# Kernel tuning notes

Measured on AMD Instinct MI355X. Metric: run time of the kernel, lower is better.

## Reference

```python
import jax, jax.numpy as jnp
import numpy as np

N_NODES = 50000
N_EDGES = 1600000
IN_DIM, HIDDEN, OUT_DIM = 128, 128, 64


def setup_inputs() -> dict:
    key = jax.random.key(0)
    ks = jax.random.split(key, 8)
    x = jax.random.normal(ks[0], (N_NODES, IN_DIM), dtype=jnp.float32)
    edge_index = jax.random.randint(ks[1], (2, N_EDGES), 0, N_NODES, dtype=jnp.int64)
    # SAGEConv params: lin_l applied to aggregated neighbors (with bias),
    # lin_r applied to root/self features (no bias) -- PyG defaults.
    def lin_init(k, fan_in, fan_out):
        bound = 1.0 / np.sqrt(fan_in)
        return jax.random.uniform(k, (fan_in, fan_out), jnp.float32, -bound, bound)
    W1_l = lin_init(ks[2], IN_DIM, HIDDEN)
    W1_r = lin_init(ks[3], IN_DIM, HIDDEN)
    b1 = jnp.zeros((HIDDEN,), jnp.float32)
    W2_l = lin_init(ks[4], HIDDEN, OUT_DIM)
    W2_r = lin_init(ks[5], HIDDEN, OUT_DIM)
    b2 = jnp.zeros((OUT_DIM,), jnp.float32)
    return {"x": x, "edge_index": edge_index, "W1_l": W1_l, "W1_r": W1_r,
            "b1": b1, "W2_l": W2_l, "W2_r": W2_r, "b2": b2}


def _sage_conv(h, src, dst, n_nodes, W_l, W_r, b):
    # gather messages from source nodes, mean-aggregate at destinations
    msg = h[src]                                              # [E, D]
    agg_sum = jax.ops.segment_sum(msg, dst, num_segments=n_nodes)
    deg = jax.ops.segment_sum(jnp.ones((src.shape[0],), h.dtype), dst,
                              num_segments=n_nodes)
    agg_mean = agg_sum / jnp.maximum(deg, 1.0)[:, None]       # [N, D]
    return agg_mean @ W_l + h @ W_r + b


def reference(x, edge_index, W1_l, W1_r, b1, W2_l, W2_r, b2):
    n = x.shape[0]
    src, dst = edge_index[0], edge_index[1]
    h = jax.nn.relu(_sage_conv(x, src, dst, n, W1_l, W1_r, b1))
    return _sage_conv(h, src, dst, n, W2_l, W2_r, b2)
```

## Files before the change

kernel.cpp:

```cpp
#include <hip/hip_runtime.h>

#define NN 50000
#define NE 1600000
#define BSTRIDE 96
#define BNODES 50
#define C_BKT 1000
#define P1_BLKS 256
#define P1_CHUNK 6250
#define ZID 50000
#define XCVT_BLKS 1563
#define WCVT_BLKS 48
#define PP_PREP (XCVT_BLKS + WCVT_BLKS)
#define RGRP 3128

typedef __bf16 bf16x8 __attribute__((ext_vector_type(8)));
typedef float  f32x4  __attribute__((ext_vector_type(4)));
typedef float  f32x2  __attribute__((ext_vector_type(2)));

__device__ __forceinline__ float bfLo(uint u) { union { uint i; float f; } v; v.i = u << 16; return v.f; }
__device__ __forceinline__ float bfHi(uint u) { union { uint i; float f; } v; v.i = u & 0xffff0000u; return v.f; }
__device__ __forceinline__ ushort f2bf(float f) {
    union { float f; uint i; } v; v.f = f;
    uint r = v.i + 0x7fffu + ((v.i >> 16) & 1u);
    return (ushort)(r >> 16);
}
__device__ __forceinline__ uint pack2(float a, float b) {
    return (uint)f2bf(a) | ((uint)f2bf(b) << 16);
}
__device__ __forceinline__ bf16x8 load8(const ushort* p) {
    union { uint4 u; bf16x8 b; } v; v.u = *(const uint4*)p; return v.b;
}

#define ACC8(u) { a0 += bfLo(u.x); a1 += bfHi(u.x); a2 += bfLo(u.y); a3 += bfHi(u.y); \
                  a4 += bfLo(u.z); a5 += bfHi(u.z); a6 += bfLo(u.w); a7 += bfHi(u.w); }

#define CVA(u, o) { f32x2 p0 = __builtin_amdgcn_cvt_pk_f32_fp8((int)(u), 0); \
                    f32x2 p1 = __builtin_amdgcn_cvt_pk_f32_fp8((int)(u), 1); \
                    a[(o)+0] += p0.x; a[(o)+1] += p0.y; a[(o)+2] += p1.x; a[(o)+3] += p1.y; }
#define ACCF8(v) { CVA((v).x, 0); CVA((v).y, 4); CVA((v).z, 8); CVA((v).w, 12); }

__device__ __forceinline__ int pkOff(int n, int k) {
    return (((n >> 4) * 4 + (k >> 5)) * 512) + (((k >> 3) & 3) * 128) + ((n & 15) * 8) + (k & 7);
}

__global__ __launch_bounds__(1024) void k_pp(
    const float4* __restrict__ x, ushort* __restrict__ xbp, uint* __restrict__ xf8,
    const float* __restrict__ W1l, const float* __restrict__ W1r,
    const float* __restrict__ W2l, const float* __restrict__ W2r,
    ushort* __restrict__ T1l, ushort* __restrict__ T1r,
    ushort* __restrict__ T2l, ushort* __restrict__ T2r,
    const int* __restrict__ src, const int* __restrict__ dst,
    uint* __restrict__ cells, uint* __restrict__ offc, ushort* __restrict__ hW) {
    __shared__ uint hist[C_BKT + 1];
    __shared__ uint part[128];
    const int b = blockIdx.x;
    const int tid = threadIdx.x;
    if (b < XCVT_BLKS) {
        int i = b * 1024 + tid;
        if (i < NN * 128 / 4) {
            float4 v = x[i];
            int r = i >> 5, k0 = (i & 31) * 4;
            ushort4 o; o.x = f2bf(v.x); o.y = f2bf(v.y); o.z = f2bf(v.z); o.w = f2bf(v.w);
            *(ushort4*)(xbp + pkOff(r, k0)) = o;
            uint rr = (uint)__builtin_amdgcn_cvt_pk_fp8_f32(v.x, v.y, 0, 0);
            rr = (uint)__builtin_amdgcn_cvt_pk_fp8_f32(v.z, v.w, (int)rr, 1);
            xf8[i] = rr;
        } else if (b == XCVT_BLKS - 1) {
            if (tid >= 512 && tid < 544) xf8[(size_t)ZID * 32 + (tid - 512)] = 0;
            else if (tid >= 544 && tid < 576) ((uint*)hW)[(size_t)ZID * 32 + (tid - 544)] = 0;
        }
    } else if (b < PP_PREP) {
        int i = (b - XCVT_BLKS) * 1024 + tid;
        if (i < 16384) {
            int k = i >> 7, n = i & 127; T1l[pkOff(n, k)] = f2bf(W1l[i]);
        } else if (i < 32768) {
            int j = i - 16384; int k = j >> 7, n = j & 127; T1r[pkOff(n, k)] = f2bf(W1r[j]);
        } else if (i < 40960) {
            int j = i - 32768; int k = j >> 6, n = j & 63;  T2l[pkOff(n, k)] = f2bf(W2l[j]);
        } else {
            int j = i - 40960; int k = j >> 6, n = j & 63;  T2r[pkOff(n, k)] = f2bf(W2r[j]);
        }
    } else {
        const int b2 = b - PP_PREP;
        for (int i = tid; i < C_BKT; i += 1024) hist[i] = 0;
        __syncthreads();
        const int beg = b2 * P1_CHUNK;
        for (int i = beg + tid; i < beg + P1_CHUNK; i += 1024)
            atomicAdd(&hist[dst[i] / BNODES], 1);
        __syncthreads();
        if (tid < 125) {
            uint s = 0;
            #pragma unroll
            for (int k = 0; k < 8; k++) {
                uint t = hist[tid * 8 + k];
                hist[tid * 8 + k] = s;
                s += t;
            }
            part[tid] = s;
        }
        __syncthreads();
        if (tid == 0) {
            uint run = 0;
            for (int t = 0; t < 125; t++) { uint tmp = part[t]; part[t] = run; run += tmp; }
        }
        __syncthreads();
        if (tid < 125) {
            uint bs = part[tid];
            if (bs) {
                #pragma unroll
                for (int k = 0; k < 8; k++) hist[tid * 8 + k] += bs;
            }
        }
        __syncthreads();
        for (int c = tid; c < C_BKT; c += 1024) {
            uint st = hist[c];
            uint en = (c == C_BKT - 1) ? (uint)P1_CHUNK : hist[c + 1];
            offc[(size_t)c * P1_BLKS + b2] = st | ((en - st) << 16);
        }
        __syncthreads();
        uint* myCells = cells + (size_t)b2 * P1_CHUNK;
        for (int i = beg + tid; i < beg + P1_CHUNK; i += 1024) {
            int d = dst[i];
            int s = src[i];
            int c = d / BNODES;
            uint p = atomicAdd(&hist[c], 1);
            myCells[p] = ((uint)(d - c * BNODES) << 16) | (uint)s;
        }
    }
}

__global__ __launch_bounds__(512) void k_pagg(
    const uint* __restrict__ cells, const uint* __restrict__ offc,
    const uchar* __restrict__ xf8, ushort* __restrict__ col,
    int* __restrict__ deg, ushort* __restrict__ aggp) {
    __shared__ uint hist[BNODES];
    __shared__ __align__(16) ushort colS[BNODES * BSTRIDE];
    const int bid = blockIdx.x;
    const int c = (bid & 7) * 125 + (bid >> 3);
    const int tid = threadIdx.x;
    if (tid < BNODES) hist[tid] = 0;
    __syncthreads();
    {
        const int b = tid >> 1, sub = tid & 1;
        uint v = offc[(size_t)c * P1_BLKS + b];
        int st = (int)(v & 0xFFFF), n = (int)(v >> 16);
        const uint* cell = cells + (size_t)b * P1_CHUNK + st;
        for (int j = sub; j < n; j += 2) {
            uint e = cell[j];
            int dl = e >> 16;
            uint p = atomicAdd(&hist[dl], 1);
            if (p < BSTRIDE) colS[dl * BSTRIDE + p] = (ushort)(e & 0xFFFF);
        }
    }
    __syncthreads();
    const int nodeBase = c * BNODES;
    if (tid < BNODES) {
        deg[nodeBase + tid] = (int)hist[tid];
        int dd = min((int)hist[tid], BSTRIDE);
        int dr = (dd + 7) & ~7;
        for (int j = dd; j < dr; j++) colS[tid * BSTRIDE + j] = (ushort)ZID;
    }
    __syncthreads();
    {
        uint4* cg = (uint4*)(col + (size_t)nodeBase * BSTRIDE);
        const uint4* cs = (const uint4*)colS;
        for (int i = tid; i < BNODES * BSTRIDE / 8; i += 512) cg[i] = cs[i];
    }
    const int wave = tid >> 6, lane = tid & 63;
    const int q = lane >> 3;
    const int cc = lane & 7;
    for (int ln = wave; ln < BNODES; ln += 8) {
        int d = (int)hist[ln];
        int dd = min(d, BSTRIDE);
        int nb = ((dd + 7) & ~7) >> 3;
        const int base = ln * BSTRIDE;
        float a[16];
        #pragma unroll
        for (int i = 0; i < 16; i++) a[i] = 0.f;
        int t = 0;
        for (; t + 4 <= nb; t += 4) {
            int s0 = (int)colS[base + t * 8 + q];
            int s1 = (int)colS[base + t * 8 + 8 + q];
            int s2 = (int)colS[base + t * 8 + 16 + q];
            int s3 = (int)colS[base + t * 8 + 24 + q];
            uint4 u0 = *(const uint4*)(xf8 + (size_t)s0 * 128 + cc * 16);
            uint4 u1 = *(const uint4*)(xf8 + (size_t)s1 * 128 + cc * 16);
            uint4 u2 = *(const uint4*)(xf8 + (size_t)s2 * 128 + cc * 16);
            uint4 u3 = *(const uint4*)(xf8 + (size_t)s3 * 128 + cc * 16);
            ACCF8(u0); ACCF8(u1); ACCF8(u2); ACCF8(u3);
        }
        for (; t < nb; t++) {
            int s = (int)colS[base + t * 8 + q];
            uint4 u = *(const uint4*)(xf8 + (size_t)s * 128 + cc * 16);
            ACCF8(u);
        }
        #pragma unroll
        for (int m = 8; m < 64; m <<= 1) {
            #pragma unroll
            for (int i = 0; i < 16; i++) a[i] += __shfl_xor(a[i], m);
        }
        if (q == 0) {
            int node = nodeBase + ln;
            float inv = 1.f / fmaxf((float)d, 1.f);
            int basep = ((node >> 4) * 4 + (cc >> 1)) * 512 + ((cc & 1) * 2) * 128 + (node & 15) * 8;
            uint4 o;
            o.x = pack2(a[0] * inv, a[1] * inv);
            o.y = pack2(a[2] * inv, a[3] * inv);
            o.z = pack2(a[4] * inv, a[5] * inv);
            o.w = pack2(a[6] * inv, a[7] * inv);
            *(uint4*)(aggp + basep) = o;
            o.x = pack2(a[8] * inv, a[9] * inv);
            o.y = pack2(a[10] * inv, a[11] * inv);
            o.z = pack2(a[12] * inv, a[13] * inv);
            o.w = pack2(a[14] * inv, a[15] * inv);
            *(uint4*)(aggp + basep + 128) = o;
        }
    }
}

#define PAD1 136
__global__ __launch_bounds__(256) void k_gemm12(
    const ushort* __restrict__ aggp, const ushort* __restrict__ xbp,
    const ushort* __restrict__ T1l, const ushort* __restrict__ T1r,
    const ushort* __restrict__ T2l, const ushort* __restrict__ T2r,
    const float* __restrict__ b1, const float* __restrict__ b2,
    ushort* __restrict__ hW, float* __restrict__ outp) {
    __shared__ ushort hS[2][16 * PAD1];
    const int lane = threadIdx.x & 63;
    const int wave = threadIdx.x >> 6;
    const int s = wave >> 1;
    const int ch = wave & 1;
    const int quad = lane >> 4, r16 = lane & 15;
    const int row0 = blockIdx.x * 32 + s * 16;
    const int g = blockIdx.x * 2 + s;
    ushort* myS = &hS[s][0];

    f32x4 acc[4];
    #pragma unroll
    for (int nt = 0; nt < 4; nt++) acc[nt] = (f32x4){0.f, 0.f, 0.f, 0.f};
    #pragma unroll
    for (int kt = 0; kt < 4; kt++) {
        bf16x8 aAgg = load8(aggp + (size_t)(g * 4 + kt) * 512 + lane * 8);
        bf16x8 aXb  = load8(xbp  + (size_t)(g * 4 + kt) * 512 + lane * 8);
        #pragma unroll
        for (int nt = 0; nt < 4; nt++) {
            const int tile = ((ch * 4 + nt) * 4 + kt) * 512 + lane * 8;
            acc[nt] = __builtin_amdgcn_mfma_f32_16x16x32_bf16(aAgg, load8(T1l + tile), acc[nt], 0, 0, 0);
            acc[nt] = __builtin_amdgcn_mfma_f32_16x16x32_bf16(aXb,  load8(T1r + tile), acc[nt], 0, 0, 0);
        }
    }
    #pragma unroll
    for (int nt = 0; nt < 4; nt++) {
        int cc = ch * 64 + nt * 16 + r16;
        float bv = b1[cc];
        #pragma unroll
        for (int i = 0; i < 4; i++)
            myS[(quad * 4 + i) * PAD1 + cc] = f2bf(fmaxf(acc[nt][i] + bv, 0.f));
    }
    __syncthreads();

    f32x4 acc2[2], acc3[2];
    #pragma unroll
    for (int nt = 0; nt < 2; nt++) {
        acc2[nt] = (f32x4){0.f, 0.f, 0.f, 0.f};
        acc3[nt] = (f32x4){0.f, 0.f, 0.f, 0.f};
    }
    #pragma unroll
    for (int kt = 0; kt < 4; kt++) {
        bf16x8 ah = load8(&myS[r16 * PAD1 + kt * 32 + quad * 8]);
        #pragma unroll
        for (int nt = 0; nt < 2; nt++) {
            const int tile = ((ch * 2 + nt) * 4 + kt) * 512 + lane * 8;
            acc2[nt] = __builtin_amdgcn_mfma_f32_16x16x32_bf16(ah, load8(T2l + tile), acc2[nt], 0, 0, 0);
            acc3[nt] = __builtin_amdgcn_mfma_f32_16x16x32_bf16(ah, load8(T2r + tile), acc3[nt], 0, 0, 0);
        }
    }
    #pragma unroll
    for (int nt = 0; nt < 2; nt++) {
        int cc = ch * 32 + nt * 16 + r16;
        float bv = b2[cc];
        #pragma unroll
        for (int i = 0; i < 4; i++) {
            int rr = row0 + quad * 4 + i;
            if (rr < NN) {
                hW[(size_t)rr * 64 + cc] = f2bf(acc2[nt][i]);
                outp[(size_t)rr * 64 + cc] = acc3[nt][i] + bv;
            }
        }
    }
}

__global__ __launch_bounds__(256) void k_agg64f(
    const ushort* __restrict__ hW, const ushort* __restrict__ col,
    const int* __restrict__ deg, const float* __restrict__ outp,
    float* __restrict__ out) {
    __shared__ __align__(16) ushort colB[4 * BSTRIDE];
    const int tid = threadIdx.x;
    const int node0 = blockIdx.x * 4;
    if (tid < 48) {
        const uint4* cg = (const uint4*)(col + (size_t)node0 * BSTRIDE);
        *(uint4*)&colB[tid * 8] = cg[tid];
    }
    __syncthreads();
    const int wave = tid >> 6, lane = tid & 63;
    const int node = node0 + wave;
    const int q = lane >> 3;
    const int c = lane & 7;
    const int base = wave * BSTRIDE;
    int d = deg[node];
    int dd = min(d, BSTRIDE);
    int nb = ((dd + 7) & ~7) >> 3;
    float a0=0.f,a1=0.f,a2=0.f,a3=0.f,a4=0.f,a5=0.f,a6=0.f,a7=0.f;
    int t = 0;
    for (; t + 4 <= nb; t += 4) {
        int s0 = (int)colB[base + t * 8 + q];
        int s1 = (int)colB[base + t * 8 + 8 + q];
        int s2 = (int)colB[base + t * 8 + 16 + q];
        int s3 = (int)colB[base + t * 8 + 24 + q];
        uint4 u0 = *(const uint4*)(hW + (size_t)s0 * 64 + c * 8);
        uint4 u1 = *(const uint4*)(hW + (size_t)s1 * 64 + c * 8);
        uint4 u2 = *(const uint4*)(hW + (size_t)s2 * 64 + c * 8);
        uint4 u3 = *(const uint4*)(hW + (size_t)s3 * 64 + c * 8);
        ACC8(u0); ACC8(u1); ACC8(u2); ACC8(u3);
    }
    for (; t < nb; t++) {
        int s = (int)colB[base + t * 8 + q];
        uint4 u = *(const uint4*)(hW + (size_t)s * 64 + c * 8);
        ACC8(u);
    }
    #pragma unroll
    for (int m = 8; m < 64; m <<= 1) {
        a0 += __shfl_xor(a0, m); a1 += __shfl_xor(a1, m);
        a2 += __shfl_xor(a2, m); a3 += __shfl_xor(a3, m);
        a4 += __shfl_xor(a4, m); a5 += __shfl_xor(a5, m);
        a6 += __shfl_xor(a6, m); a7 += __shfl_xor(a7, m);
    }
    if (q == 0) {
        float inv = 1.f / fmaxf((float)d, 1.f);
        float4 p0 = *(const float4*)(outp + (size_t)node * 64 + c * 8);
        float4 p1 = *(const float4*)(outp + (size_t)node * 64 + c * 8 + 4);
        float4 o;
        o.x = a0 * inv + p0.x; o.y = a1 * inv + p0.y;
        o.z = a2 * inv + p0.z; o.w = a3 * inv + p0.w;
        *(float4*)(out + (size_t)node * 64 + c * 8) = o;
        o.x = a4 * inv + p1.x; o.y = a5 * inv + p1.y;
        o.z = a6 * inv + p1.z; o.w = a7 * inv + p1.w;
        *(float4*)(out + (size_t)node * 64 + c * 8 + 4) = o;
    }
}

extern "C" void kernel_launch(void* const* d_in, const int* in_sizes, int n_in,
                              void* d_out, int out_size, void* d_ws, size_t ws_size,
                              hipStream_t stream) {
    const float* x   = (const float*)d_in[0];
    const int*   ei  = (const int*)d_in[1];
    const float* W1l = (const float*)d_in[2];
    const float* W1r = (const float*)d_in[3];
    const float* b1  = (const float*)d_in[4];
    const float* W2l = (const float*)d_in[5];
    const float* W2r = (const float*)d_in[6];
    const float* b2  = (const float*)d_in[7];
    float* out = (float*)d_out;

    const int* src = ei;
    const int* dst = ei + NE;

    char* w = (char*)d_ws;
    ushort* col   = (ushort*)w;                  w += (size_t)NN * BSTRIDE * 2;
    int* deg      = (int*)w;                     w += (size_t)50048 * 4;
    uint* offc    = (uint*)w;                    w += (size_t)C_BKT * P1_BLKS * 4;
    ushort* xbp   = (ushort*)w;                  w += (size_t)RGRP * 2048 * 2;
    ushort* T1l   = (ushort*)w;                  w += 128 * 128 * 2;
    ushort* T1r   = (ushort*)w;                  w += 128 * 128 * 2;
    ushort* T2l   = (ushort*)w;                  w += 64 * 128 * 2;
    ushort* T2r   = (ushort*)w;                  w += 64 * 128 * 2;
    ushort* aggp  = (ushort*)w;                  w += (size_t)RGRP * 2048 * 2;
    ushort* hW    = (ushort*)w;                  w += (size_t)(NN + 16) * 64 * 2;
    float* outp   = (float*)w;                   w += (size_t)NN * 64 * 4;
    uchar* xf8    = (uchar*)w;                   w += (size_t)(NN + 16) * 128;
    uint* cells   = (uint*)w;                    w += (size_t)NE * 4;

    k_pp<<<PP_PREP + P1_BLKS, 1024, 0, stream>>>(
        (const float4*)x, xbp, (uint*)xf8, W1l, W1r, W2l, W2r,
        T1l, T1r, T2l, T2r, src, dst, cells, offc, hW);

    k_pagg<<<C_BKT, 512, 0, stream>>>(cells, offc, xf8, col, deg, aggp);

    k_gemm12<<<(NN + 31) / 32, 256, 0, stream>>>(aggp, xbp, T1l, T1r, T2l, T2r, b1, b2, hW, outp);

    k_agg64f<<<NN / 4, 256, 0, stream>>>(hW, col, deg, outp, out);
}
```

Baseline: 196.0 us.

## Halve aggregation bucket size and use packed f32x2 accumulation

Buckets now cover 25 destination nodes instead of 50, giving 2000 aggregation blocks of 256 threads instead of 1000 blocks of 512. Each thread now scans one partition's cell range serially instead of two threads splitting it. The bucket prefix scan is widened to match. Separately, the bf16 and fp8 accumulators in both aggregation kernels are rewritten as f32x2 vector adds so the compiler can emit packed FP32 adds. The trade is more blocks and a larger offset table against less work per block and fewer add instructions.

```diff
diff --git a/kernel.cpp b/kernel.cpp
--- a/kernel.cpp
+++ b/kernel.cpp
@@ -3,8 +3,8 @@
 #define NN 50000
 #define NE 1600000
 #define BSTRIDE 96
-#define BNODES 50
-#define C_BKT 1000
+#define BNODES 25
+#define C_BKT 2000
 #define P1_BLKS 256
 #define P1_CHUNK 6250
 #define ZID 50000
@@ -19,6 +19,9 @@
 
 __device__ __forceinline__ float bfLo(uint u) { union { uint i; float f; } v; v.i = u << 16; return v.f; }
 __device__ __forceinline__ float bfHi(uint u) { union { uint i; float f; } v; v.i = u & 0xffff0000u; return v.f; }
+__device__ __forceinline__ f32x2 bfPair(uint u) {
+    union { uint i[2]; f32x2 f; } v; v.i[0] = u << 16; v.i[1] = u & 0xffff0000u; return v.f;
+}
 __device__ __forceinline__ ushort f2bf(float f) {
     union { float f; uint i; } v; v.f = f;
     uint r = v.i + 0x7fffu + ((v.i >> 16) & 1u);
@@ -31,13 +34,12 @@
     union { uint4 u; bf16x8 b; } v; v.u = *(const uint4*)p; return v.b;
 }
 
-#define ACC8(u) { a0 += bfLo(u.x); a1 += bfHi(u.x); a2 += bfLo(u.y); a3 += bfHi(u.y); \
-                  a4 += bfLo(u.z); a5 += bfHi(u.z); a6 += bfLo(u.w); a7 += bfHi(u.w); }
+#define ACC8P(u) { b0 += bfPair(u.x); b1 += bfPair(u.y); b2 += bfPair(u.z); b3 += bfPair(u.w); }
 
 #define CVA(u, o) { f32x2 p0 = __builtin_amdgcn_cvt_pk_f32_fp8((int)(u), 0); \
                     f32x2 p1 = __builtin_amdgcn_cvt_pk_f32_fp8((int)(u), 1); \
-                    a[(o)+0] += p0.x; a[(o)+1] += p0.y; a[(o)+2] += p1.x; a[(o)+3] += p1.y; }
-#define ACCF8(v) { CVA((v).x, 0); CVA((v).y, 4); CVA((v).z, 8); CVA((v).w, 12); }
+                    a[(o)] += p0; a[(o)+1] += p1; }
+#define ACCF8(v) { CVA((v).x, 0); CVA((v).y, 2); CVA((v).z, 4); CVA((v).w, 6); }
 
 __device__ __forceinline__ int pkOff(int n, int k) {
     return (((n >> 4) * 4 + (k >> 5)) * 512) + (((k >> 3) & 3) * 128) + ((n & 15) * 8) + (k & 7);
@@ -52,7 +54,7 @@
     const int* __restrict__ src, const int* __restrict__ dst,
     uint* __restrict__ cells, uint* __restrict__ offc, ushort* __restrict__ hW) {
     __shared__ uint hist[C_BKT + 1];
-    __shared__ uint part[128];
+    __shared__ uint part[250];
     const int b = blockIdx.x;
     const int tid = threadIdx.x;
     if (b < XCVT_BLKS) {
@@ -88,7 +90,7 @@
         for (int i = beg + tid; i < beg + P1_CHUNK; i += 1024)
             atomicAdd(&hist[dst[i] / BNODES], 1);
         __syncthreads();
-        if (tid < 125) {
+        if (tid < 250) {
             uint s = 0;
             #pragma unroll
             for (int k = 0; k < 8; k++) {
@@ -101,10 +103,10 @@
         __syncthreads();
         if (tid == 0) {
             uint run = 0;
-            for (int t = 0; t < 125; t++) { uint tmp = part[t]; part[t] = run; run += tmp; }
-        }
-        __syncthreads();
-        if (tid < 125) {
+            for (int t = 0; t < 250; t++) { uint tmp = part[t]; part[t] = run; run += tmp; }
+        }
+        __syncthreads();
+        if (tid < 250) {
             uint bs = part[tid];
             if (bs) {
                 #pragma unroll
@@ -129,23 +131,22 @@
     }
 }
 
-__global__ __launch_bounds__(512) void k_pagg(
+__global__ __launch_bounds__(256) void k_pagg(
     const uint* __restrict__ cells, const uint* __restrict__ offc,
     const uchar* __restrict__ xf8, ushort* __restrict__ col,
     int* __restrict__ deg, ushort* __restrict__ aggp) {
     __shared__ uint hist[BNODES];
     __shared__ __align__(16) ushort colS[BNODES * BSTRIDE];
     const int bid = blockIdx.x;
-    const int c = (bid & 7) * 125 + (bid >> 3);
+    const int c = (bid & 7) * 250 + (bid >> 3);
     const int tid = threadIdx.x;
     if (tid < BNODES) hist[tid] = 0;
     __syncthreads();
     {
-        const int b = tid >> 1, sub = tid & 1;
-        uint v = offc[(size_t)c * P1_BLKS + b];
+        uint v = offc[(size_t)c * P1_BLKS + tid];
         int st = (int)(v & 0xFFFF), n = (int)(v >> 16);
-        const uint* cell = cells + (size_t)b * P1_CHUNK + st;
-        for (int j = sub; j < n; j += 2) {
+        const uint* cell = cells + (size_t)tid * P1_CHUNK + st;
+        for (int j = 0; j < n; j++) {
             uint e = cell[j];
             int dl = e >> 16;
             uint p = atomicAdd(&hist[dl], 1);
@@ -164,19 +165,19 @@
     {
         uint4* cg = (uint4*)(col + (size_t)nodeBase * BSTRIDE);
         const uint4* cs = (const uint4*)colS;
-        for (int i = tid; i < BNODES * BSTRIDE / 8; i += 512) cg[i] = cs[i];
+        for (int i = tid; i < BNODES * BSTRIDE / 8; i += 256) cg[i] = cs[i];
     }
     const int wave = tid >> 6, lane = tid & 63;
     const int q = lane >> 3;
     const int cc = lane & 7;
-    for (int ln = wave; ln < BNODES; ln += 8) {
+    for (int ln = wave; ln < BNODES; ln += 4) {
         int d = (int)hist[ln];
         int dd = min(d, BSTRIDE);
         int nb = ((dd + 7) & ~7) >> 3;
         const int base = ln * BSTRIDE;
-        float a[16];
-        #pragma unroll
-        for (int i = 0; i < 16; i++) a[i] = 0.f;
+        f32x2 a[8];
+        #pragma unroll
+        for (int i = 0; i < 8; i++) a[i] = (f32x2){0.f, 0.f};
         int t = 0;
         for (; t + 4 <= nb; t += 4) {
             int s0 = (int)colS[base + t * 8 + q];
@@ -197,22 +198,29 @@
         #pragma unroll
         for (int m = 8; m < 64; m <<= 1) {
             #pragma unroll
-            for (int i = 0; i < 16; i++) a[i] += __shfl_xor(a[i], m);
+            for (int i = 0; i < 8; i++) {
+                f32x2 t2;
+                t2.x = __shfl_xor(a[i].x, m);
+                t2.y = __shfl_xor(a[i].y, m);
+                a[i] += t2;
+            }
         }
         if (q == 0) {
             int node = nodeBase + ln;
             float inv = 1.f / fmaxf((float)d, 1.f);
+            #pragma unroll
+            for (int i = 0; i < 8; i++) a[i] *= inv;
             int basep = ((node >> 4) * 4 + (cc >> 1)) * 512 + ((cc & 1) * 2) * 128 + (node & 15) * 8;
             uint4 o;
-            o.x = pack2(a[0] * inv, a[1] * inv);
-            o.y = pack2(a[2] * inv, a[3] * inv);
-            o.z = pack2(a[4] * inv, a[5] * inv);
-            o.w = pack2(a[6] * inv, a[7] * inv);
+            o.x = pack2(a[0].x, a[0].y);
+            o.y = pack2(a[1].x, a[1].y);
+            o.z = pack2(a[2].x, a[2].y);
+            o.w = pack2(a[3].x, a[3].y);
             *(uint4*)(aggp + basep) = o;
-            o.x = pack2(a[8] * inv, a[9] * inv);
-            o.y = pack2(a[10] * inv, a[11] * inv);
-            o.z = pack2(a[12] * inv, a[13] * inv);
-            o.w = pack2(a[14] * inv, a[15] * inv);
+            o.x = pack2(a[4].x, a[4].y);
+            o.y = pack2(a[5].x, a[5].y);
+            o.z = pack2(a[6].x, a[6].y);
+            o.w = pack2(a[7].x, a[7].y);
             *(uint4*)(aggp + basep + 128) = o;
         }
     }
@@ -310,7 +318,7 @@
     int d = deg[node];
     int dd = min(d, BSTRIDE);
     int nb = ((dd + 7) & ~7) >> 3;
-    float a0=0.f,a1=0.f,a2=0.f,a3=0.f,a4=0.f,a5=0.f,a6=0.f,a7=0.f;
+    f32x2 b0 = {0.f,0.f}, b1 = {0.f,0.f}, b2 = {0.f,0.f}, b3 = {0.f,0.f};
     int t = 0;
     for (; t + 4 <= nb; t += 4) {
         int s0 = (int)colB[base + t * 8 + q];
@@ -321,30 +329,32 @@
         uint4 u1 = *(const uint4*)(hW + (size_t)s1 * 64 + c * 8);
         uint4 u2 = *(const uint4*)(hW + (size_t)s2 * 64 + c * 8);
         uint4 u3 = *(const uint4*)(hW + (size_t)s3 * 64 + c * 8);
-        ACC8(u0); ACC8(u1); ACC8(u2); ACC8(u3);
+        ACC8P(u0); ACC8P(u1); ACC8P(u2); ACC8P(u3);
     }
     for (; t < nb; t++) {
         int s = (int)colB[base + t * 8 + q];
         uint4 u = *(const uint4*)(hW + (size_t)s * 64 + c * 8);
-        ACC8(u);
+        ACC8P(u);
     }
     #pragma unroll
     for (int m = 8; m < 64; m <<= 1) {
-        a0 += __shfl_xor(a0, m); a1 += __shfl_xor(a1, m);
-        a2 += __shfl_xor(a2, m); a3 += __shfl_xor(a3, m);
-        a4 += __shfl_xor(a4, m); a5 += __shfl_xor(a5, m);
-        a6 += __shfl_xor(a6, m); a7 += __shfl_xor(a7, m);
+        f32x2 t0, t1, t2, t3;
+        t0.x = __shfl_xor(b0.x, m); t0.y = __shfl_xor(b0.y, m);
+        t1.x = __shfl_xor(b1.x, m); t1.y = __shfl_xor(b1.y, m);
+        t2.x = __shfl_xor(b2.x, m); t2.y = __shfl_xor(b2.y, m);
+        t3.x = __shfl_xor(b3.x, m); t3.y = __shfl_xor(b3.y, m);
+        b0 += t0; b1 += t1; b2 += t2; b3 += t3;
     }
     if (q == 0) {
         float inv = 1.f / fmaxf((float)d, 1.f);
         float4 p0 = *(const float4*)(outp + (size_t)node * 64 + c * 8);
         float4 p1 = *(const float4*)(outp + (size_t)node * 64 + c * 8 + 4);
         float4 o;
-        o.x = a0 * inv + p0.x; o.y = a1 * inv + p0.y;
-        o.z = a2 * inv + p0.z; o.w = a3 * inv + p0.w;
+        o.x = b0.x * inv + p0.x; o.y = b0.y * inv + p0.y;
+        o.z = b1.x * inv + p0.z; o.w = b1.y * inv + p0.w;
         *(float4*)(out + (size_t)node * 64 + c * 8) = o;
-        o.x = a4 * inv + p1.x; o.y = a5 * inv + p1.y;
-        o.z = a6 * inv + p1.z; o.w = a7 * inv + p1.w;
+        o.x = b2.x * inv + p1.x; o.y = b2.y * inv + p1.y;
+        o.z = b3.x * inv + p1.z; o.w = b3.y * inv + p1.w;
         *(float4*)(out + (size_t)node * 64 + c * 8 + 4) = o;
     }
 }
@@ -384,7 +394,7 @@
         (const float4*)x, xbp, (uint*)xf8, W1l, W1r, W2l, W2r,
         T1l, T1r, T2l, T2r, src, dst, cells, offc, hW);
 
-    k_pagg<<<C_BKT, 512, 0, stream>>>(cells, offc, xf8, col, deg, aggp);
+    k_pagg<<<C_BKT, 256, 0, stream>>>(cells, offc, xf8, col, deg, aggp);
 
     k_gemm12<<<(NN + 31) / 32, 256, 0, stream>>>(aggp, xbp, T1l, T1r, T2l, T2r, b1, b2, hW, outp);
 
```

Result: slower. 201.9 us (+3.0%).

## Process two destination nodes per wave in gather kernels with packed float2 accumulation

Applied to the files above, without the earlier changes.

Both aggregation kernels now have each wave handle two destination nodes at once, interleaving their neighbor gathers. Shorter lists are padded with the zero row so the two streams share one loop, and accumulation uses packed float2 vectors. The edge-bucketing loop in k_pagg is unrolled by two, and the XCD-interleaved block-to-bucket mapping is removed. The intent is more memory-level parallelism per wave and packed FP32 adds. In exchange, unequal degrees cause wasted loads of the zero row, register pressure rises, and k_agg64f launches half as many blocks.

```diff
diff --git a/kernel.cpp b/kernel.cpp
--- a/kernel.cpp
+++ b/kernel.cpp
@@ -17,8 +17,9 @@
 typedef float  f32x4  __attribute__((ext_vector_type(4)));
 typedef float  f32x2  __attribute__((ext_vector_type(2)));
 
-__device__ __forceinline__ float bfLo(uint u) { union { uint i; float f; } v; v.i = u << 16; return v.f; }
-__device__ __forceinline__ float bfHi(uint u) { union { uint i; float f; } v; v.i = u & 0xffff0000u; return v.f; }
+__device__ __forceinline__ f32x2 bfPair(uint u) {
+    union { uint i[2]; f32x2 f; } v; v.i[0] = u << 16; v.i[1] = u & 0xffff0000u; return v.f;
+}
 __device__ __forceinline__ ushort f2bf(float f) {
     union { float f; uint i; } v; v.f = f;
     uint r = v.i + 0x7fffu + ((v.i >> 16) & 1u);
@@ -31,13 +32,12 @@
     union { uint4 u; bf16x8 b; } v; v.u = *(const uint4*)p; return v.b;
 }
 
-#define ACC8(u) { a0 += bfLo(u.x); a1 += bfHi(u.x); a2 += bfLo(u.y); a3 += bfHi(u.y); \
-                  a4 += bfLo(u.z); a5 += bfHi(u.z); a6 += bfLo(u.w); a7 += bfHi(u.w); }
-
-#define CVA(u, o) { f32x2 p0 = __builtin_amdgcn_cvt_pk_f32_fp8((int)(u), 0); \
-                    f32x2 p1 = __builtin_amdgcn_cvt_pk_f32_fp8((int)(u), 1); \
-                    a[(o)+0] += p0.x; a[(o)+1] += p0.y; a[(o)+2] += p1.x; a[(o)+3] += p1.y; }
-#define ACCF8(v) { CVA((v).x, 0); CVA((v).y, 4); CVA((v).z, 8); CVA((v).w, 12); }
+#define CVA(A, u, o) { f32x2 p0 = __builtin_amdgcn_cvt_pk_f32_fp8((int)(u), 0); \
+                       f32x2 p1 = __builtin_amdgcn_cvt_pk_f32_fp8((int)(u), 1); \
+                       A[(o)] += p0; A[(o)+1] += p1; }
+#define ACCF8(A, v) { CVA(A, (v).x, 0); CVA(A, (v).y, 2); CVA(A, (v).z, 4); CVA(A, (v).w, 6); }
+
+#define ACC8P(A, u) { A[0] += bfPair(u.x); A[1] += bfPair(u.y); A[2] += bfPair(u.z); A[3] += bfPair(u.w); }
 
 __device__ __forceinline__ int pkOff(int n, int k) {
     return (((n >> 4) * 4 + (k >> 5)) * 512) + (((k >> 3) & 3) * 128) + ((n & 15) * 8) + (k & 7);
@@ -59,9 +59,9 @@
         int i = b * 1024 + tid;
         if (i < NN * 128 / 4) {
             float4 v = x[i];
-            int r = i >> 5, k0 = (i & 31) * 4;
+            int r = i >> 5, j = i & 31;
             ushort4 o; o.x = f2bf(v.x); o.y = f2bf(v.y); o.z = f2bf(v.z); o.w = f2bf(v.w);
-            *(ushort4*)(xbp + pkOff(r, k0)) = o;
+            *(ushort4*)(xbp + pkOff(r, j * 4)) = o;
             uint rr = (uint)__builtin_amdgcn_cvt_pk_fp8_f32(v.x, v.y, 0, 0);
             rr = (uint)__builtin_amdgcn_cvt_pk_fp8_f32(v.z, v.w, (int)rr, 1);
             xf8[i] = rr;
@@ -135,8 +135,7 @@
     int* __restrict__ deg, ushort* __restrict__ aggp) {
     __shared__ uint hist[BNODES];
     __shared__ __align__(16) ushort colS[BNODES * BSTRIDE];
-    const int bid = blockIdx.x;
-    const int c = (bid & 7) * 125 + (bid >> 3);
+    const int c = blockIdx.x;
     const int tid = threadIdx.x;
     if (tid < BNODES) hist[tid] = 0;
     __syncthreads();
@@ -145,9 +144,19 @@
         uint v = offc[(size_t)c * P1_BLKS + b];
         int st = (int)(v & 0xFFFF), n = (int)(v >> 16);
         const uint* cell = cells + (size_t)b * P1_CHUNK + st;
-        for (int j = sub; j < n; j += 2) {
+        int j = sub * 2;
+        for (; j + 1 < n; j += 4) {
+            uint e0 = cell[j];
+            uint e1 = cell[j + 1];
+            int dl0 = (int)(e0 >> 16), dl1 = (int)(e1 >> 16);
+            uint p0 = atomicAdd(&hist[dl0], 1);
+            uint p1 = atomicAdd(&hist[dl1], 1);
+            if (p0 < BSTRIDE) colS[dl0 * BSTRIDE + p0] = (ushort)(e0 & 0xFFFF);
+            if (p1 < BSTRIDE) colS[dl1 * BSTRIDE + p1] = (ushort)(e1 & 0xFFFF);
+        }
+        if (j < n) {
             uint e = cell[j];
-            int dl = e >> 16;
+            int dl = (int)(e >> 16);
             uint p = atomicAdd(&hist[dl], 1);
             if (p < BSTRIDE) colS[dl * BSTRIDE + p] = (ushort)(e & 0xFFFF);
         }
@@ -169,51 +178,73 @@
     const int wave = tid >> 6, lane = tid & 63;
     const int q = lane >> 3;
     const int cc = lane & 7;
-    for (int ln = wave; ln < BNODES; ln += 8) {
-        int d = (int)hist[ln];
-        int dd = min(d, BSTRIDE);
-        int nb = ((dd + 7) & ~7) >> 3;
-        const int base = ln * BSTRIDE;
-        float a[16];
-        #pragma unroll
-        for (int i = 0; i < 16; i++) a[i] = 0.f;
-        int t = 0;
-        for (; t + 4 <= nb; t += 4) {
-            int s0 = (int)colS[base + t * 8 + q];
-            int s1 = (int)colS[base + t * 8 + 8 + q];
-            int s2 = (int)colS[base + t * 8 + 16 + q];
-            int s3 = (int)colS[base + t * 8 + 24 + q];
-            uint4 u0 = *(const uint4*)(xf8 + (size_t)s0 * 128 + cc * 16);
-            uint4 u1 = *(const uint4*)(xf8 + (size_t)s1 * 128 + cc * 16);
-            uint4 u2 = *(const uint4*)(xf8 + (size_t)s2 * 128 + cc * 16);
-            uint4 u3 = *(const uint4*)(xf8 + (size_t)s3 * 128 + cc * 16);
-            ACCF8(u0); ACCF8(u1); ACCF8(u2); ACCF8(u3);
-        }
-        for (; t < nb; t++) {
-            int s = (int)colS[base + t * 8 + q];
-            uint4 u = *(const uint4*)(xf8 + (size_t)s * 128 + cc * 16);
-            ACCF8(u);
+    for (int ln = wave; ln < BNODES; ln += 16) {
+        const int lnB = ln + 8;
+        const bool hasB = (lnB < BNODES);
+        int dA = (int)hist[ln];
+        int dB = hasB ? (int)hist[lnB] : 0;
+        int nbA = ((min(dA, BSTRIDE) + 7) & ~7) >> 3;
+        int nbB = ((min(dB, BSTRIDE) + 7) & ~7) >> 3;
+        int nbM = max(nbA, nbB);
+        const int baseA = ln * BSTRIDE;
+        const int baseB = lnB * BSTRIDE;
+        f32x2 a[8], bb[8];
+        #pragma unroll
+        for (int i = 0; i < 8; i++) { a[i] = (f32x2){0.f, 0.f}; bb[i] = (f32x2){0.f, 0.f}; }
+        for (int t = 0; t < nbM; t += 2) {
+            int sA0 = (t     < nbA) ? (int)colS[baseA + t * 8 + q]       : ZID;
+            int sA1 = (t + 1 < nbA) ? (int)colS[baseA + (t + 1) * 8 + q] : ZID;
+            int sB0 = (t     < nbB) ? (int)colS[baseB + t * 8 + q]       : ZID;
+            int sB1 = (t + 1 < nbB) ? (int)colS[baseB + (t + 1) * 8 + q] : ZID;
+            uint4 uA0 = *(const uint4*)(xf8 + (size_t)sA0 * 128 + cc * 16);
+            uint4 uA1 = *(const uint4*)(xf8 + (size_t)sA1 * 128 + cc * 16);
+            uint4 uB0 = *(const uint4*)(xf8 + (size_t)sB0 * 128 + cc * 16);
+            uint4 uB1 = *(const uint4*)(xf8 + (size_t)sB1 * 128 + cc * 16);
+            ACCF8(a, uA0); ACCF8(a, uA1); ACCF8(bb, uB0); ACCF8(bb, uB1);
         }
         #pragma unroll
         for (int m = 8; m < 64; m <<= 1) {
             #pragma unroll
-            for (int i = 0; i < 16; i++) a[i] += __shfl_xor(a[i], m);
+            for (int i = 0; i < 8; i++) {
+                f32x2 tA, tB;
+                tA.x = __shfl_xor(a[i].x, m);  tA.y = __shfl_xor(a[i].y, m);
+                tB.x = __shfl_xor(bb[i].x, m); tB.y = __shfl_xor(bb[i].y, m);
+                a[i] += tA; bb[i] += tB;
+            }
         }
         if (q == 0) {
-            int node = nodeBase + ln;
-            float inv = 1.f / fmaxf((float)d, 1.f);
-            int basep = ((node >> 4) * 4 + (cc >> 1)) * 512 + ((cc & 1) * 2) * 128 + (node & 15) * 8;
-            uint4 o;
-            o.x = pack2(a[0] * inv, a[1] * inv);
-            o.y = pack2(a[2] * inv, a[3] * inv);
-            o.z = pack2(a[4] * inv, a[5] * inv);
-            o.w = pack2(a[6] * inv, a[7] * inv);
-            *(uint4*)(aggp + basep) = o;
-            o.x = pack2(a[8] * inv, a[9] * inv);
-            o.y = pack2(a[10] * inv, a[11] * inv);
-            o.z = pack2(a[12] * inv, a[13] * inv);
-            o.w = pack2(a[14] * inv, a[15] * inv);
-            *(uint4*)(aggp + basep + 128) = o;
+            {
+                int node = nodeBase + ln;
+                float inv = 1.f / fmaxf((float)dA, 1.f);
+                int basep = ((node >> 4) * 4 + (cc >> 1)) * 512 + ((cc & 1) * 2) * 128 + (node & 15) * 8;
+                uint4 o;
+                o.x = pack2(a[0].x * inv, a[0].y * inv);
+                o.y = pack2(a[1].x * inv, a[1].y * inv);
+                o.z = pack2(a[2].x * inv, a[2].y * inv);
+                o.w = pack2(a[3].x * inv, a[3].y * inv);
+                *(uint4*)(aggp + basep) = o;
+                o.x = pack2(a[4].x * inv, a[4].y * inv);
+                o.y = pack2(a[5].x * inv, a[5].y * inv);
+                o.z = pack2(a[6].x * inv, a[6].y * inv);
+                o.w = pack2(a[7].x * inv, a[7].y * inv);
+                *(uint4*)(aggp + basep + 128) = o;
+            }
+            if (hasB) {
+                int node = nodeBase + lnB;
+                float inv = 1.f / fmaxf((float)dB, 1.f);
+                int basep = ((node >> 4) * 4 + (cc >> 1)) * 512 + ((cc & 1) * 2) * 128 + (node & 15) * 8;
+                uint4 o;
+                o.x = pack2(bb[0].x * inv, bb[0].y * inv);
+                o.y = pack2(bb[1].x * inv, bb[1].y * inv);
+                o.z = pack2(bb[2].x * inv, bb[2].y * inv);
+                o.w = pack2(bb[3].x * inv, bb[3].y * inv);
+                *(uint4*)(aggp + basep) = o;
+                o.x = pack2(bb[4].x * inv, bb[4].y * inv);
+                o.y = pack2(bb[5].x * inv, bb[5].y * inv);
+                o.z = pack2(bb[6].x * inv, bb[6].y * inv);
+                o.w = pack2(bb[7].x * inv, bb[7].y * inv);
+                *(uint4*)(aggp + basep + 128) = o;
+            }
         }
     }
 }
@@ -294,58 +325,75 @@
     const ushort* __restrict__ hW, const ushort* __restrict__ col,
     const int* __restrict__ deg, const float* __restrict__ outp,
     float* __restrict__ out) {
-    __shared__ __align__(16) ushort colB[4 * BSTRIDE];
+    __shared__ __align__(16) ushort colB[8 * BSTRIDE];
     const int tid = threadIdx.x;
-    const int node0 = blockIdx.x * 4;
-    if (tid < 48) {
+    const int node0 = blockIdx.x * 8;
+    if (tid < 96) {
         const uint4* cg = (const uint4*)(col + (size_t)node0 * BSTRIDE);
         *(uint4*)&colB[tid * 8] = cg[tid];
     }
     __syncthreads();
     const int wave = tid >> 6, lane = tid & 63;
-    const int node = node0 + wave;
+    const int nodeA = node0 + wave;
+    const int nodeB = node0 + wave + 4;
     const int q = lane >> 3;
     const int c = lane & 7;
-    const int base = wave * BSTRIDE;
-    int d = deg[node];
-    int dd = min(d, BSTRIDE);
-    int nb = ((dd + 7) & ~7) >> 3;
-    float a0=0.f,a1=0.f,a2=0.f,a3=0.f,a4=0.f,a5=0.f,a6=0.f,a7=0.f;
-    int t = 0;
-    for (; t + 4 <= nb; t += 4) {
-        int s0 = (int)colB[base + t * 8 + q];
-        int s1 = (int)colB[base + t * 8 + 8 + q];
-        int s2 = (int)colB[base + t * 8 + 16 + q];
-        int s3 = (int)colB[base + t * 8 + 24 + q];
-        uint4 u0 = *(const uint4*)(hW + (size_t)s0 * 64 + c * 8);
-        uint4 u1 = *(const uint4*)(hW + (size_t)s1 * 64 + c * 8);
-        uint4 u2 = *(const uint4*)(hW + (size_t)s2 * 64 + c * 8);
-        uint4 u3 = *(const uint4*)(hW + (size_t)s3 * 64 + c * 8);
-        ACC8(u0); ACC8(u1); ACC8(u2); ACC8(u3);
-    }
-    for (; t < nb; t++) {
-        int s = (int)colB[base + t * 8 + q];
-        uint4 u = *(const uint4*)(hW + (size_t)s * 64 + c * 8);
-        ACC8(u);
+    const int baseA = wave * BSTRIDE;
+    const int baseB = (wave + 4) * BSTRIDE;
+    int dA = deg[nodeA];
+    int dB = deg[nodeB];
+    int nbA = ((min(dA, BSTRIDE) + 7) & ~7) >> 3;
+    int nbB = ((min(dB, BSTRIDE) + 7) & ~7) >> 3;
+    int nbM = max(nbA, nbB);
+    f32x2 a4[4], b4[4];
+    #pragma unroll
+    for (int i = 0; i < 4; i++) { a4[i] = (f32x2){0.f, 0.f}; b4[i] = (f32x2){0.f, 0.f}; }
+    for (int t = 0; t < nbM; t += 2) {
+        int sA0 = (t     < nbA) ? (int)colB[baseA + t * 8 + q]       : ZID;
+        int sA1 = (t + 1 < nbA) ? (int)colB[baseA + (t + 1) * 8 + q] : ZID;
+        int sB0 = (t     < nbB) ? (int)colB[baseB + t * 8 + q]       : ZID;
+        int sB1 = (t + 1 < nbB) ? (int)colB[baseB + (t + 1) * 8 + q] : ZID;
+        uint4 uA0 = *(const uint4*)(hW + (size_t)sA0 * 64 + c * 8);
+        uint4 uA1 = *(const uint4*)(hW + (size_t)sA1 * 64 + c * 8);
+        uint4 uB0 = *(const uint4*)(hW + (size_t)sB0 * 64 + c * 8);
+        uint4 uB1 = *(const uint4*)(hW + (size_t)sB1 * 64 + c * 8);
+        ACC8P(a4, uA0); ACC8P(a4, uA1); ACC8P(b4, uB0); ACC8P(b4, uB1);
     }
     #pragma unroll
     for (int m = 8; m < 64; m <<= 1) {
-        a0 += __shfl_xor(a0, m); a1 += __shfl_xor(a1, m);
-        a2 += __shfl_xor(a2, m); a3 += __shfl_xor(a3, m);
-        a4 += __shfl_xor(a4, m); a5 += __shfl_xor(a5, m);
-        a6 += __shfl_xor(a6, m); a7 += __shfl_xor(a7, m);
+        #pragma unroll
+        for (int i = 0; i < 4; i++) {
+            f32x2 tA, tB;
+            tA.x = __shfl_xor(a4[i].x, m); tA.y = __shfl_xor(a4[i].y, m);
+            tB.x = __shfl_xor(b4[i].x, m); tB.y = __shfl_xor(b4[i].y, m);
+            a4[i] += tA; b4[i] += tB;
+        }
     }
     if (q == 0) {
-        float inv = 1.f / fmaxf((float)d, 1.f);
-        float4 p0 = *(const float4*)(outp + (size_t)node * 64 + c * 8);
-        float4 p1 = *(const float4*)(outp + (size_t)node * 64 + c * 8 + 4);
-        float4 o;
-        o.x = a0 * inv + p0.x; o.y = a1 * inv + p0.y;
-        o.z = a2 * inv + p0.z; o.w = a3 * inv + p0.w;
-        *(float4*)(out + (size_t)node * 64 + c * 8) = o;
-        o.x = a4 * inv + p1.x; o.y = a5 * inv + p1.y;
-        o.z = a6 * inv + p1.z; o.w = a7 * inv + p1.w;
-        *(float4*)(out + (size_t)node * 64 + c * 8 + 4) = o;
+        {
+            float inv = 1.f / fmaxf((float)dA, 1.f);
+            float4 p0 = *(const float4*)(outp + (size_t)nodeA * 64 + c * 8);
+            float4 p1 = *(const float4*)(outp + (size_t)nodeA * 64 + c * 8 + 4);
+            float4 o;
+            o.x = a4[0].x * inv + p0.x; o.y = a4[0].y * inv + p0.y;
+            o.z = a4[1].x * inv + p0.z; o.w = a4[1].y * inv + p0.w;
+            *(float4*)(out + (size_t)nodeA * 64 + c * 8) = o;
+            o.x = a4[2].x * inv + p1.x; o.y = a4[2].y * inv + p1.y;
+            o.z = a4[3].x * inv + p1.z; o.w = a4[3].y * inv + p1.w;
+            *(float4*)(out + (size_t)nodeA * 64 + c * 8 + 4) = o;
+        }
+        {
+            float inv = 1.f / fmaxf((float)dB, 1.f);
+            float4 p0 = *(const float4*)(outp + (size_t)nodeB * 64 + c * 8);
+            float4 p1 = *(const float4*)(outp + (size_t)nodeB * 64 + c * 8 + 4);
+            float4 o;
+            o.x = b4[0].x * inv + p0.x; o.y = b4[0].y * inv + p0.y;
+            o.z = b4[1].x * inv + p0.z; o.w = b4[1].y * inv + p0.w;
+            *(float4*)(out + (size_t)nodeB * 64 + c * 8) = o;
+            o.x = b4[2].x * inv + p1.x; o.y = b4[2].y * inv + p1.y;
+            o.z = b4[3].x * inv + p1.z; o.w = b4[3].y * inv + p1.w;
+            *(float4*)(out + (size_t)nodeB * 64 + c * 8 + 4) = o;
+        }
     }
 }
 
@@ -388,5 +436,5 @@
 
     k_gemm12<<<(NN + 31) / 32, 256, 0, stream>>>(aggp, xbp, T1l, T1r, T2l, T2r, b1, b2, hW, outp);
 
-    k_agg64f<<<NN / 4, 256, 0, stream>>>(hW, col, deg, outp, out);
-}
+    k_agg64f<<<NN / 8, 256, 0, stream>>>(hW, col, deg, outp, out);
+}
```

Result: slower. 201.6 us (+2.8%).
